# Performance work log

Hardware: AMD Instinct MI355X
Metric: run time of the kernel (lower is better)

## Reference

```python
import jax, jax.numpy as jnp
import numpy as np


def setup_inputs() -> dict:
    key = jax.random.key(0)
    k1, k2, k3 = jax.random.split(key, 3)
    B, H, W = 32, 512, 512
    N = H * W  # tokens
    K = 32768  # positive_trials
    decision_scores = jax.random.normal(k1, (B, N, 2), dtype=jnp.float32)
    s_map = jax.random.uniform(k2, (B, 1, H, W), dtype=jnp.float32)
    # uniform noise for gumbel sampling, kept away from {0,1} for log stability
    u = jax.random.uniform(k3, (B, N, 2), dtype=jnp.float32, minval=1e-6, maxval=1.0 - 1e-6)
    return {"decision_scores": decision_scores, "s_map": s_map, "u": u, "positive_trials": K}


def reference(decision_scores, s_map, u, positive_trials):
    B, N, _ = decision_scores.shape
    # gumbel_softmax(hard=False, tau=1): softmax(logits + gumbel_noise)
    gumbel = -jnp.log(-jnp.log(u))
    logp = jax.nn.log_softmax(decision_scores + gumbel, axis=-1)  # [B, N, 2]
    # soft_decisions = p[..., 0]
    # Tokenizer: [B, 1, H, W] -> [B, N, 1]; use channel 0 as salience score.
    scores = s_map.reshape(B, 1, -1).transpose(0, 2, 1)[..., 0]  # [B, N]
    # argsort descending, take top-k indices == lax.top_k indices
    _, idx = jax.lax.top_k(scores, positive_trials)  # [B, K]
    trials = jnp.zeros((B, N), dtype=decision_scores.dtype)
    trials = trials.at[jnp.arange(B)[:, None], idx].set(1.0)  # scatter ones
    # BCE(sum): -sum(t*log(p) + (1-t)*log(1-p)); with 2-class softmax, 1-p0 = p1.
    # torch BCE clamps log terms at -100.
    logp0 = jnp.clip(logp[..., 0], -100.0)
    logp1 = jnp.clip(logp[..., 1], -100.0)
    loss = -jnp.sum(trials * logp0 + (1.0 - trials) * logp1)
    return loss
```

## Files before the change

### kernel.cpp

```cpp
#include <hip/hip_runtime.h>

#define NB    4096
#define CAP   4096
#define BATCH 32
#define NTOK  262144
#define LOSS_BLOCKS 8192

__device__ __forceinline__ int bucket_of(float v) {
    int b = (int)(v * (float)NB);
    return b > NB - 1 ? NB - 1 : b;
}

__global__ void hist_kernel(const float* __restrict__ smap, int* __restrict__ hist) {
    __shared__ int lh[NB];
    for (int i = threadIdx.x; i < NB; i += blockDim.x) lh[i] = 0;
    __syncthreads();
    const int cbpb = 8;
    int b  = blockIdx.x / cbpb;
    int cb = blockIdx.x % cbpb;
    const int chunk = NTOK / cbpb;
    const float4* src = (const float4*)(smap + (size_t)b * NTOK + (size_t)cb * chunk);
    const int nf4 = chunk / 4;
    for (int i = threadIdx.x; i < nf4; i += blockDim.x) {
        float4 v = src[i];
        atomicAdd(&lh[bucket_of(v.x)], 1);
        atomicAdd(&lh[bucket_of(v.y)], 1);
        atomicAdd(&lh[bucket_of(v.z)], 1);
        atomicAdd(&lh[bucket_of(v.w)], 1);
    }
    __syncthreads();
    int* gh = hist + b * NB;
    for (int i = threadIdx.x; i < NB; i += blockDim.x) {
        int c = lh[i];
        if (c) atomicAdd(&gh[i], c);
    }
}

__global__ void select_kernel(const int* __restrict__ hist, const int* __restrict__ kptr,
                              int* __restrict__ tbR) {
    int b = blockIdx.x;
    const int* gh = hist + b * NB;
    __shared__ int h[NB];
    __shared__ int csum[256];
    __shared__ int above[256];
    int t = threadIdx.x;
    const int C = NB / 256;
    int base = t * C;
    int s = 0;
    for (int i = 0; i < C; i++) { int v = gh[base + i]; h[base + i] = v; s += v; }
    csum[t] = s;
    __syncthreads();
    if (t == 0) {
        int acc = 0;
        for (int c = 255; c >= 0; c--) { above[c] = acc; acc += csum[c]; }
    }
    __syncthreads();
    int K = *kptr;
    int cum = above[t];
    for (int i = C - 1; i >= 0; i--) {
        int hb = h[base + i];
        if (cum < K && cum + hb >= K) {
            tbR[2 * b]     = base + i;
            tbR[2 * b + 1] = K - cum;
        }
        cum += hb;
    }
}

__global__ void collect_kernel(const float* __restrict__ smap, const int* __restrict__ tbR,
                               int* __restrict__ cnt, float* __restrict__ cval,
                               int* __restrict__ cidx) {
    const int cbpb = 64;
    int b  = blockIdx.x / cbpb;
    int cb = blockIdx.x % cbpb;
    const int chunk = NTOK / cbpb;
    int tb = tbR[2 * b];
    const float4* src = (const float4*)(smap + (size_t)b * NTOK + (size_t)cb * chunk);
    const int nf4 = chunk / 4;
    int base_n = cb * chunk;
    for (int i = threadIdx.x; i < nf4; i += blockDim.x) {
        float4 v = src[i];
        float vals[4] = {v.x, v.y, v.z, v.w};
#pragma unroll
        for (int s = 0; s < 4; s++) {
            if (bucket_of(vals[s]) == tb) {
                int p = atomicAdd(&cnt[b], 1);
                if (p < CAP) {
                    cval[b * CAP + p] = vals[s];
                    cidx[b * CAP + p] = base_n + 4 * i + s;
                }
            }
        }
    }
}

__global__ void refine_kernel(const int* __restrict__ tbR, const int* __restrict__ cnt,
                              const float* __restrict__ cval, const int* __restrict__ cidx,
                              float* __restrict__ T, int* __restrict__ ncut) {
    int b = blockIdx.x;
    int R = tbR[2 * b + 1];
    int M = cnt[b];
    bool overflow = (M > CAP);
    if (M > CAP) M = CAP;
    __shared__ float sv[CAP];
    __shared__ int   si[CAP];
    for (int i = threadIdx.x; i < M; i += blockDim.x) {
        sv[i] = cval[b * CAP + i];
        si[i] = cidx[b * CAP + i];
    }
    __syncthreads();
    if (overflow || R > M || R < 1) {
        if (threadIdx.x == 0) { T[b] = (float)tbR[2 * b] / (float)NB; ncut[b] = 0x7fffffff; }
        return;
    }
    for (int i = threadIdx.x; i < M; i += blockDim.x) {
        float vi = sv[i]; int ii = si[i];
        int r = 0;
        for (int j = 0; j < M; j++) {
            float vj = sv[j];
            r += (vj > vi) || (vj == vi && si[j] < ii);
        }
        if (r == R - 1) { T[b] = vi; ncut[b] = ii; }
    }
}

__device__ __forceinline__ float token_loss(float d0, float d1, float u0, float u1,
                                            bool sel) {
    float g0 = -__logf(-__logf(u0));
    float g1 = -__logf(-__logf(u1));
    float dd = (d0 + g0) - (d1 + g1);
    float l  = __logf(1.f + __expf(-fabsf(dd)));
    float lp0 = (dd >= 0.f) ? -l      : dd - l;
    float lp1 = (dd >= 0.f) ? -l - dd : -l;
    lp0 = fmaxf(lp0, -100.f); lp1 = fmaxf(lp1, -100.f);
    return sel ? -lp0 : -lp1;
}

__global__ void loss_kernel(const float* __restrict__ ds, const float* __restrict__ u,
                            const float* __restrict__ smap, const float* __restrict__ T,
                            const int* __restrict__ ncut, float* __restrict__ partials) {
    int tid = blockIdx.x * blockDim.x + threadIdx.x;
    int b = tid >> 16;
    int p = tid & 65535;
    const float4* ds4 = (const float4*)(ds + (size_t)b * NTOK * 2);
    const float4* u4  = (const float4*)(u  + (size_t)b * NTOK * 2);
    const float4* s4  = (const float4*)(smap + (size_t)b * NTOK);
    float4 dA = ds4[2 * p];
    float4 dB = ds4[2 * p + 1];
    float4 uA = u4[2 * p];
    float4 uB = u4[2 * p + 1];
    float4 sv = s4[p];
    float Tb = T[b];
    int   nc = ncut[b];
    int   n0 = p << 2;

    bool s0 = (sv.x > Tb) || (sv.x == Tb && (n0 + 0) <= nc);
    bool s1 = (sv.y > Tb) || (sv.y == Tb && (n0 + 1) <= nc);
    bool s2 = (sv.z > Tb) || (sv.z == Tb && (n0 + 2) <= nc);
    bool s3 = (sv.w > Tb) || (sv.w == Tb && (n0 + 3) <= nc);

    float acc = token_loss(dA.x, dA.y, uA.x, uA.y, s0)
              + token_loss(dA.z, dA.w, uA.z, uA.w, s1)
              + token_loss(dB.x, dB.y, uB.x, uB.y, s2)
              + token_loss(dB.z, dB.w, uB.z, uB.w, s3);

    for (int off = 32; off > 0; off >>= 1) acc += __shfl_down(acc, off, 64);
    __shared__ float red[4];
    int lane = threadIdx.x & 63, wv = threadIdx.x >> 6;
    if (lane == 0) red[wv] = acc;
    __syncthreads();
    if (threadIdx.x == 0)
        partials[blockIdx.x] = red[0] + red[1] + red[2] + red[3];
}

__global__ void reduce_kernel(const float* __restrict__ partials, float* __restrict__ out) {
    float acc = 0.f;
    for (int i = threadIdx.x; i < LOSS_BLOCKS; i += blockDim.x) acc += partials[i];
    for (int off = 32; off > 0; off >>= 1) acc += __shfl_down(acc, off, 64);
    __shared__ float red[16];
    int lane = threadIdx.x & 63, wv = threadIdx.x >> 6;
    if (lane == 0) red[wv] = acc;
    __syncthreads();
    if (threadIdx.x == 0) {
        float s = 0.f;
        for (int w = 0; w < (int)(blockDim.x >> 6); w++) s += red[w];
        out[0] = s;
    }
}

extern "C" void kernel_launch(void* const* d_in, const int* in_sizes, int n_in,
                              void* d_out, int out_size, void* d_ws, size_t ws_size,
                              hipStream_t stream) {
    const float* ds   = (const float*)d_in[0];
    const float* smap = (const float*)d_in[1];
    const float* u    = (const float*)d_in[2];
    const int*   kptr = (const int*)d_in[3];

    int*   hist = (int*)d_ws;
    int*   cnt  = hist + BATCH * NB;
    int*   tbR  = cnt + BATCH;
    float* T    = (float*)(tbR + 2 * BATCH);
    int*   ncut = (int*)(T + BATCH);
    float* cval = (float*)(ncut + BATCH);
    int*   cidx = (int*)(cval + BATCH * CAP);
    float* partials = (float*)(cidx + BATCH * CAP);

    hipMemsetAsync(hist, 0, (size_t)(BATCH * NB + BATCH) * sizeof(int), stream);

    hist_kernel<<<256, 1024, 0, stream>>>(smap, hist);
    select_kernel<<<BATCH, 256, 0, stream>>>(hist, kptr, tbR);
    collect_kernel<<<2048, 256, 0, stream>>>(smap, tbR, cnt, cval, cidx);
    refine_kernel<<<BATCH, 256, 0, stream>>>(tbR, cnt, cval, cidx, T, ncut);
    loss_kernel<<<LOSS_BLOCKS, 256, 0, stream>>>(ds, u, smap, T, ncut, partials);
    reduce_kernel<<<1, 1024, 0, stream>>>(partials, (float*)d_out);
}
```

Before: 208.6 us.

## Fuse histogram, select, collect, refine into one per-batch kernel; fold final reduction

Merges the histogram, threshold-bucket selection, candidate collection and rank refinement into a single kernel that runs one 1024-thread block per batch, keeping the histogram and candidates in shared memory. This removes the memset, the global atomics and several launches. The loss kernel now processes eight tokens per thread using a strided layout, and the last block to finish performs the final reduction, found through an atomic counter, which drops the separate reduce kernel. In exchange, selection runs on only 32 blocks, so each block scans its full batch twice with limited parallelism, and the candidate cap is smaller, which makes the overflow fallback more likely.

```diff
diff --git a/kernel.cpp b/kernel.cpp
--- a/kernel.cpp
+++ b/kernel.cpp
@@ -1,124 +1,94 @@
 #include <hip/hip_runtime.h>
 
 #define NB    4096
-#define CAP   4096
+#define CAPL  1024
 #define BATCH 32
 #define NTOK  262144
-#define LOSS_BLOCKS 8192
+#define LOSS_BLOCKS 4096
+#define LOSS_THREADS 256
 
 __device__ __forceinline__ int bucket_of(float v) {
     int b = (int)(v * (float)NB);
     return b > NB - 1 ? NB - 1 : b;
 }
 
-__global__ void hist_kernel(const float* __restrict__ smap, int* __restrict__ hist) {
-    __shared__ int lh[NB];
-    for (int i = threadIdx.x; i < NB; i += blockDim.x) lh[i] = 0;
+__global__ __launch_bounds__(1024) void select_kernel(
+        const float* __restrict__ smap, const int* __restrict__ kptr,
+        float* __restrict__ T, int* __restrict__ ncut, int* __restrict__ done) {
+    __shared__ int   lh[NB];
+    __shared__ int   suf[1024 + 1];
+    __shared__ float cv[CAPL];
+    __shared__ int   ci[CAPL];
+    __shared__ int   s_cnt, s_tb, s_R;
+    const int b = blockIdx.x;
+    const int t = threadIdx.x;
+    if (t == 0) { s_cnt = 0; if (b == 0) *done = 0; }
+    for (int i = t; i < NB; i += 1024) lh[i] = 0;
     __syncthreads();
-    const int cbpb = 8;
-    int b  = blockIdx.x / cbpb;
-    int cb = blockIdx.x % cbpb;
-    const int chunk = NTOK / cbpb;
-    const float4* src = (const float4*)(smap + (size_t)b * NTOK + (size_t)cb * chunk);
-    const int nf4 = chunk / 4;
-    for (int i = threadIdx.x; i < nf4; i += blockDim.x) {
-        float4 v = src[i];
+
+    const float4* src = (const float4*)(smap + (size_t)b * NTOK);
+    #pragma unroll 4
+    for (int k = 0; k < 64; k++) {
+        float4 v = src[t + k * 1024];
         atomicAdd(&lh[bucket_of(v.x)], 1);
         atomicAdd(&lh[bucket_of(v.y)], 1);
         atomicAdd(&lh[bucket_of(v.z)], 1);
         atomicAdd(&lh[bucket_of(v.w)], 1);
     }
     __syncthreads();
-    int* gh = hist + b * NB;
-    for (int i = threadIdx.x; i < NB; i += blockDim.x) {
-        int c = lh[i];
-        if (c) atomicAdd(&gh[i], c);
+
+    const int base = t * 4;
+    int c = lh[base] + lh[base + 1] + lh[base + 2] + lh[base + 3];
+    suf[t] = c;
+    if (t == 0) suf[1024] = 0;
+    __syncthreads();
+    for (int off = 1; off < 1024; off <<= 1) {
+        int v = suf[t] + ((t + off < 1024) ? suf[t + off] : 0);
+        __syncthreads();
+        suf[t] = v;
+        __syncthreads();
     }
-}
-
-__global__ void select_kernel(const int* __restrict__ hist, const int* __restrict__ kptr,
-                              int* __restrict__ tbR) {
-    int b = blockIdx.x;
-    const int* gh = hist + b * NB;
-    __shared__ int h[NB];
-    __shared__ int csum[256];
-    __shared__ int above[256];
-    int t = threadIdx.x;
-    const int C = NB / 256;
-    int base = t * C;
-    int s = 0;
-    for (int i = 0; i < C; i++) { int v = gh[base + i]; h[base + i] = v; s += v; }
-    csum[t] = s;
-    __syncthreads();
-    if (t == 0) {
-        int acc = 0;
-        for (int c = 255; c >= 0; c--) { above[c] = acc; acc += csum[c]; }
+    const int K = *kptr;
+    {
+        int cum = suf[t + 1];
+        #pragma unroll
+        for (int i = 3; i >= 0; i--) {
+            int hb = lh[base + i];
+            if (cum < K && cum + hb >= K) { s_tb = base + i; s_R = K - cum; }
+            cum += hb;
+        }
     }
     __syncthreads();
-    int K = *kptr;
-    int cum = above[t];
-    for (int i = C - 1; i >= 0; i--) {
-        int hb = h[base + i];
-        if (cum < K && cum + hb >= K) {
-            tbR[2 * b]     = base + i;
-            tbR[2 * b + 1] = K - cum;
-        }
-        cum += hb;
-    }
-}
+    const int tb = s_tb;
 
-__global__ void collect_kernel(const float* __restrict__ smap, const int* __restrict__ tbR,
-                               int* __restrict__ cnt, float* __restrict__ cval,
-                               int* __restrict__ cidx) {
-    const int cbpb = 64;
-    int b  = blockIdx.x / cbpb;
-    int cb = blockIdx.x % cbpb;
-    const int chunk = NTOK / cbpb;
-    int tb = tbR[2 * b];
-    const float4* src = (const float4*)(smap + (size_t)b * NTOK + (size_t)cb * chunk);
-    const int nf4 = chunk / 4;
-    int base_n = cb * chunk;
-    for (int i = threadIdx.x; i < nf4; i += blockDim.x) {
-        float4 v = src[i];
+    #pragma unroll 4
+    for (int k = 0; k < 64; k++) {
+        int fi = t + k * 1024;
+        float4 v = src[fi];
         float vals[4] = {v.x, v.y, v.z, v.w};
-#pragma unroll
+        #pragma unroll
         for (int s = 0; s < 4; s++) {
             if (bucket_of(vals[s]) == tb) {
-                int p = atomicAdd(&cnt[b], 1);
-                if (p < CAP) {
-                    cval[b * CAP + p] = vals[s];
-                    cidx[b * CAP + p] = base_n + 4 * i + s;
-                }
+                int p = atomicAdd(&s_cnt, 1);
+                if (p < CAPL) { cv[p] = vals[s]; ci[p] = 4 * fi + s; }
             }
         }
     }
-}
+    __syncthreads();
 
-__global__ void refine_kernel(const int* __restrict__ tbR, const int* __restrict__ cnt,
-                              const float* __restrict__ cval, const int* __restrict__ cidx,
-                              float* __restrict__ T, int* __restrict__ ncut) {
-    int b = blockIdx.x;
-    int R = tbR[2 * b + 1];
-    int M = cnt[b];
-    bool overflow = (M > CAP);
-    if (M > CAP) M = CAP;
-    __shared__ float sv[CAP];
-    __shared__ int   si[CAP];
-    for (int i = threadIdx.x; i < M; i += blockDim.x) {
-        sv[i] = cval[b * CAP + i];
-        si[i] = cidx[b * CAP + i];
-    }
-    __syncthreads();
+    int M = s_cnt, R = s_R;
+    bool overflow = (M > CAPL);
+    if (M > CAPL) M = CAPL;
     if (overflow || R > M || R < 1) {
-        if (threadIdx.x == 0) { T[b] = (float)tbR[2 * b] / (float)NB; ncut[b] = 0x7fffffff; }
+        if (t == 0) { T[b] = (float)tb / (float)NB; ncut[b] = 0x7fffffff; }
         return;
     }
-    for (int i = threadIdx.x; i < M; i += blockDim.x) {
-        float vi = sv[i]; int ii = si[i];
+    for (int i = t; i < M; i += 1024) {
+        float vi = cv[i]; int ii = ci[i];
         int r = 0;
         for (int j = 0; j < M; j++) {
-            float vj = sv[j];
-            r += (vj > vi) || (vj == vi && si[j] < ii);
+            float vj = cv[j];
+            r += (vj > vi) || (vj == vi && ci[j] < ii);
         }
         if (r == R - 1) { T[b] = vi; ncut[b] = ii; }
     }
@@ -136,55 +106,77 @@
     return sel ? -lp0 : -lp1;
 }
 
-__global__ void loss_kernel(const float* __restrict__ ds, const float* __restrict__ u,
-                            const float* __restrict__ smap, const float* __restrict__ T,
-                            const int* __restrict__ ncut, float* __restrict__ partials) {
-    int tid = blockIdx.x * blockDim.x + threadIdx.x;
-    int b = tid >> 16;
-    int p = tid & 65535;
+__global__ __launch_bounds__(256) void loss_kernel(
+        const float* __restrict__ ds, const float* __restrict__ u,
+        const float* __restrict__ smap, const float* __restrict__ T,
+        const int* __restrict__ ncut, float* __restrict__ partials,
+        int* __restrict__ done, float* __restrict__ out) {
+    const int b = blockIdx.x >> 7;
+    const int q = ((blockIdx.x & 127) << 8) | threadIdx.x;
+    const int PSTR = 32768;
     const float4* ds4 = (const float4*)(ds + (size_t)b * NTOK * 2);
     const float4* u4  = (const float4*)(u  + (size_t)b * NTOK * 2);
-    const float4* s4  = (const float4*)(smap + (size_t)b * NTOK);
-    float4 dA = ds4[2 * p];
-    float4 dB = ds4[2 * p + 1];
-    float4 uA = u4[2 * p];
-    float4 uB = u4[2 * p + 1];
-    float4 sv = s4[p];
-    float Tb = T[b];
-    int   nc = ncut[b];
-    int   n0 = p << 2;
+    const float2* s2  = (const float2*)(smap + (size_t)b * NTOK);
+    const float Tb = T[b];
+    const int   nc = ncut[b];
 
-    bool s0 = (sv.x > Tb) || (sv.x == Tb && (n0 + 0) <= nc);
-    bool s1 = (sv.y > Tb) || (sv.y == Tb && (n0 + 1) <= nc);
-    bool s2 = (sv.z > Tb) || (sv.z == Tb && (n0 + 2) <= nc);
-    bool s3 = (sv.w > Tb) || (sv.w == Tb && (n0 + 3) <= nc);
+    float4 dA = ds4[q];            float4 dB = ds4[q + PSTR];
+    float4 dC = ds4[q + 2*PSTR];   float4 dD = ds4[q + 3*PSTR];
+    float4 uA = u4[q];             float4 uB = u4[q + PSTR];
+    float4 uC = u4[q + 2*PSTR];    float4 uD = u4[q + 3*PSTR];
+    float2 sA = s2[q];             float2 sB = s2[q + PSTR];
+    float2 sC = s2[q + 2*PSTR];    float2 sD = s2[q + 3*PSTR];
 
-    float acc = token_loss(dA.x, dA.y, uA.x, uA.y, s0)
-              + token_loss(dA.z, dA.w, uA.z, uA.w, s1)
-              + token_loss(dB.x, dB.y, uB.x, uB.y, s2)
-              + token_loss(dB.z, dB.w, uB.z, uB.w, s3);
+    float acc = 0.f;
+    {   int n = 2 * q;
+        bool a = (sA.x > Tb) || (sA.x == Tb && n     <= nc);
+        bool c = (sA.y > Tb) || (sA.y == Tb && n + 1 <= nc);
+        acc += token_loss(dA.x, dA.y, uA.x, uA.y, a)
+             + token_loss(dA.z, dA.w, uA.z, uA.w, c);
+    }
+    {   int n = 2 * (q + PSTR);
+        bool a = (sB.x > Tb) || (sB.x == Tb && n     <= nc);
+        bool c = (sB.y > Tb) || (sB.y == Tb && n + 1 <= nc);
+        acc += token_loss(dB.x, dB.y, uB.x, uB.y, a)
+             + token_loss(dB.z, dB.w, uB.z, uB.w, c);
+    }
+    {   int n = 2 * (q + 2*PSTR);
+        bool a = (sC.x > Tb) || (sC.x == Tb && n     <= nc);
+        bool c = (sC.y > Tb) || (sC.y == Tb && n + 1 <= nc);
+        acc += token_loss(dC.x, dC.y, uC.x, uC.y, a)
+             + token_loss(dC.z, dC.w, uC.z, uC.w, c);
+    }
+    {   int n = 2 * (q + 3*PSTR);
+        bool a = (sD.x > Tb) || (sD.x == Tb && n     <= nc);
+        bool c = (sD.y > Tb) || (sD.y == Tb && n + 1 <= nc);
+        acc += token_loss(dD.x, dD.y, uD.x, uD.y, a)
+             + token_loss(dD.z, dD.w, uD.z, uD.w, c);
+    }
 
     for (int off = 32; off > 0; off >>= 1) acc += __shfl_down(acc, off, 64);
     __shared__ float red[4];
-    int lane = threadIdx.x & 63, wv = threadIdx.x >> 6;
-    if (lane == 0) red[wv] = acc;
-    __syncthreads();
-    if (threadIdx.x == 0)
-        partials[blockIdx.x] = red[0] + red[1] + red[2] + red[3];
-}
-
-__global__ void reduce_kernel(const float* __restrict__ partials, float* __restrict__ out) {
-    float acc = 0.f;
-    for (int i = threadIdx.x; i < LOSS_BLOCKS; i += blockDim.x) acc += partials[i];
-    for (int off = 32; off > 0; off >>= 1) acc += __shfl_down(acc, off, 64);
-    __shared__ float red[16];
-    int lane = threadIdx.x & 63, wv = threadIdx.x >> 6;
+    __shared__ int s_last;
+    const int lane = threadIdx.x & 63, wv = threadIdx.x >> 6;
     if (lane == 0) red[wv] = acc;
     __syncthreads();
     if (threadIdx.x == 0) {
+        partials[blockIdx.x] = red[0] + red[1] + red[2] + red[3];
+        __threadfence();
+        int old = atomicAdd(done, 1);
+        s_last = (old == LOSS_BLOCKS - 1) ? 1 : 0;
+    }
+    __syncthreads();
+    if (s_last) {
+        __threadfence();
+        const int t = threadIdx.x;
         float s = 0.f;
-        for (int w = 0; w < (int)(blockDim.x >> 6); w++) s += red[w];
-        out[0] = s;
+        #pragma unroll
+        for (int j = 0; j < 16; j++) s += partials[t * 16 + j];
+        for (int off = 32; off > 0; off >>= 1) s += __shfl_down(s, off, 64);
+        __shared__ float fr[4];
+        if (lane == 0) fr[wv] = s;
+        __syncthreads();
+        if (t == 0) out[0] = fr[0] + fr[1] + fr[2] + fr[3];
     }
 }
 
@@ -196,21 +188,12 @@
     const float* u    = (const float*)d_in[2];
     const int*   kptr = (const int*)d_in[3];
 
-    int*   hist = (int*)d_ws;
-    int*   cnt  = hist + BATCH * NB;
-    int*   tbR  = cnt + BATCH;
-    float* T    = (float*)(tbR + 2 * BATCH);
-    int*   ncut = (int*)(T + BATCH);
-    float* cval = (float*)(ncut + BATCH);
-    int*   cidx = (int*)(cval + BATCH * CAP);
-    float* partials = (float*)(cidx + BATCH * CAP);
+    float* T        = (float*)d_ws;
+    int*   ncut     = (int*)(T + BATCH);
+    float* partials = (float*)(ncut + BATCH);
+    int*   done     = (int*)(partials + LOSS_BLOCKS);
 
-    hipMemsetAsync(hist, 0, (size_t)(BATCH * NB + BATCH) * sizeof(int), stream);
-
-    hist_kernel<<<256, 1024, 0, stream>>>(smap, hist);
-    select_kernel<<<BATCH, 256, 0, stream>>>(hist, kptr, tbR);
-    collect_kernel<<<2048, 256, 0, stream>>>(smap, tbR, cnt, cval, cidx);
-    refine_kernel<<<BATCH, 256, 0, stream>>>(tbR, cnt, cval, cidx, T, ncut);
-    loss_kernel<<<LOSS_BLOCKS, 256, 0, stream>>>(ds, u, smap, T, ncut, partials);
-    reduce_kernel<<<1, 1024, 0, stream>>>(partials, (float*)d_out);
+    select_kernel<<<BATCH, 1024, 0, stream>>>(smap, kptr, T, ncut, done);
+    loss_kernel<<<LOSS_BLOCKS, LOSS_THREADS, 0, stream>>>(ds, u, smap, T, ncut,
+                                                          partials, done, (float*)d_out);
 }
```

New measurement: 420.4 us. 102% more time.
